# Performance work log

Measured on AMD Instinct MI355X. Metric: run time of the kernel, lower is better.

## Reference

```python
import jax, jax.numpy as jnp
import numpy as np
import math

B, S, D, H, FF = 2, 2048, 1024, 16, 4096
HD = D // H
EPS = 1e-5


def setup_inputs() -> dict:
    key = jax.random.key(0)
    ks = jax.random.split(key, 16)
    w = lambda k, shape: (jax.random.normal(k, shape, jnp.float32) * 0.02)
    future = jnp.triu(jnp.ones((S, S), dtype=bool), k=1)
    causal_mask = jnp.where(future, -jnp.inf, 0.0).astype(jnp.float32)
    return {
        "src": jax.random.normal(ks[0], (B, S, D), jnp.float32),
        "causal_mask": causal_mask,
        "Wq": w(ks[1], (D, D)), "bq": jnp.zeros((D,), jnp.float32),
        "Wk": w(ks[2], (D, D)), "bk": jnp.zeros((D,), jnp.float32),
        "Wv": w(ks[3], (D, D)), "bv": jnp.zeros((D,), jnp.float32),
        "Wo": w(ks[4], (D, D)), "bo": jnp.zeros((D,), jnp.float32),
        "W1": w(ks[5], (D, FF)), "b1": jnp.zeros((FF,), jnp.float32),
        "W2": w(ks[6], (FF, D)), "b2": jnp.zeros((D,), jnp.float32),
        "ln1_g": jnp.ones((D,), jnp.float32), "ln1_b": jnp.zeros((D,), jnp.float32),
        "ln2_g": jnp.ones((D,), jnp.float32), "ln2_b": jnp.zeros((D,), jnp.float32),
    }


def _layernorm(x, g, b):
    mu = jnp.mean(x, axis=-1, keepdims=True)
    var = jnp.mean((x - mu) ** 2, axis=-1, keepdims=True)
    return (x - mu) * jax.lax.rsqrt(var + EPS) * g + b


def reference(src, causal_mask, Wq, bq, Wk, bk, Wv, bv, Wo, bo,
              W1, b1, W2, b2, ln1_g, ln1_b, ln2_g, ln2_b):
    # QKV projections, split heads: [B,S,D] -> [B,H,S,HD]
    def split_heads(x):
        return x.reshape(B, S, H, HD).transpose(0, 2, 1, 3)

    q = split_heads(src @ Wq + bq)
    k = split_heads(src @ Wk + bk)
    v = split_heads(src @ Wv + bv)

    # scores: [B,H,S,S]; attn_mask = causal_mask broadcast over batch, then head dim
    scores = jnp.einsum("bhqd,bhkd->bhqk", q, k) / math.sqrt(HD)
    scores = scores + causal_mask[None, None, :, :]
    # scores[scores != scores] = 0
    scores = jnp.where(jnp.isnan(scores), 0.0, scores)
    # rows that are entirely inf -> 0
    mask_all_inf = jnp.all(jnp.isinf(scores), axis=-1, keepdims=True)
    scores = jnp.where(mask_all_inf, 0.0, scores)
    attn = jax.nn.softmax(scores, axis=-1)
    attn = jnp.where(jnp.isnan(attn), 0.0, attn)

    ctx = jnp.einsum("bhqk,bhkd->bhqd", attn, v)
    ctx = ctx.transpose(0, 2, 1, 3).reshape(B, S, D)
    attn_out = ctx @ Wo + bo

    x = _layernorm(src + attn_out, ln1_g, ln1_b)
    ff = jax.nn.relu(x @ W1 + b1) @ W2 + b2
    return _layernorm(x + ff, ln2_g, ln2_b)
```

## Files before the change

### kernel.cpp

```cpp
#include <hip/hip_runtime.h>

#define SS 2048
#define DD 1024
#define HH 16
#define HDIM 64
#define BB 2
#define FFD 4096
#define MR (BB*SS)
#define QKVLD 3072

typedef __bf16 bf16;
typedef __bf16 bf16x4 __attribute__((ext_vector_type(4)));
typedef __bf16 bf16x8 __attribute__((ext_vector_type(8)));
typedef float f32x4 __attribute__((ext_vector_type(4)));

struct P4 { bf16* p[4]; };

__device__ inline f32x4 mfma32(bf16x8 a, bf16x8 b, f32x4 c) {
  return __builtin_amdgcn_mfma_f32_16x16x32_bf16(a, b, c, 0, 0, 0);
}

__device__ inline void gload_lds16(const void* g, void* l) {
  __builtin_amdgcn_global_load_lds(
      (const __attribute__((address_space(1))) void*)g,
      (__attribute__((address_space(3))) void*)l, 16, 0, 0);
}

__global__ __launch_bounds__(256)
void cvt_bf16_kernel(const float* __restrict__ in, bf16* __restrict__ out, int n) {
  int i = (blockIdx.x * 256 + threadIdx.x) * 4;
  if (i >= n) return;
  float4 v = *(const float4*)(in + i);
  bf16x4 o;
  o[0] = (bf16)v.x; o[1] = (bf16)v.y; o[2] = (bf16)v.z; o[3] = (bf16)v.w;
  *(bf16x4*)(out + i) = o;
}

__global__ __launch_bounds__(256)
void concat_bias_kernel(const float* __restrict__ bq, const float* __restrict__ bk,
                        const float* __restrict__ bv, float* __restrict__ out) {
  int i = blockIdx.x * 256 + threadIdx.x;
  out[i] = i < 1024 ? bq[i] : (i < 2048 ? bk[i - 1024] : bv[i - 2048]);
}

__global__ __launch_bounds__(256)
void transpose_w_kernel(const float* __restrict__ W, bf16* __restrict__ Wt,
                        int K, int N) {
  __shared__ float t[32][33];
  int tx = threadIdx.x & 31, ty = threadIdx.x >> 5;
  int n0 = blockIdx.x * 32, k0 = blockIdx.y * 32;
  #pragma unroll
  for (int i = 0; i < 4; ++i)
    t[ty + i*8][tx] = W[(size_t)(k0 + ty + i*8) * N + n0 + tx];
  __syncthreads();
  #pragma unroll
  for (int i = 0; i < 4; ++i)
    Wt[(size_t)(n0 + ty + i*8) * K + k0 + tx] = (bf16)t[tx][ty + i*8];
}

__global__ __launch_bounds__(256)
void transpose_v_kernel(const bf16* __restrict__ V2d, bf16* __restrict__ Vt) {
  __shared__ bf16 t[32][33];
  int tx = threadIdx.x & 31, ty = threadIdx.x >> 5;
  int s0 = blockIdx.x * 32, d0 = blockIdx.y * 32;
  int bh = blockIdx.z;
  int b = bh >> 4, h = bh & 15;
  #pragma unroll
  for (int i = 0; i < 4; ++i)
    t[ty + i*8][tx] = V2d[(size_t)(b*SS + s0 + ty + i*8) * QKVLD + h*HDIM + d0 + tx];
  __syncthreads();
  #pragma unroll
  for (int i = 0; i < 4; ++i)
    Vt[((size_t)bh*HDIM + d0 + ty + i*8) * SS + s0 + tx] = t[tx][ty + i*8];
}

template<int OUT_BF16, int RELU, int SPLITK>
__global__ __launch_bounds__(512)
void gemm256(const bf16* __restrict__ A, const bf16* __restrict__ Bt,
             const float* __restrict__ bias, void* __restrict__ Cout,
             P4 part, int Ndim, int Kdim) {
  __shared__ bf16 Asm[2][256 * 64];
  __shared__ bf16 Bsm[2][256 * 64];
  const int gx = gridDim.x, gy = gridDim.y;
  const int gxy = gx * gy;
  const int nwg = gxy * gridDim.z;
  const int lin = (blockIdx.z * gy + blockIdx.y) * gx + blockIdx.x;
  const int swz = (lin & 7) * (nwg >> 3) + (lin >> 3);
  int bz = 0, rem = swz;
  if (SPLITK > 1) { bz = swz / gxy; rem = swz - bz * gxy; }
  const int by = rem / gx, bx = rem - by * gx;
  const int m0 = by * 256, n0 = bx * 256;
  const int tid = threadIdx.x;
  const int wave = tid >> 6, lane = tid & 63;
  const int g = lane >> 4, r = lane & 15;
  const int wr = wave >> 2, wn = wave & 3;
  const int kstart = bz * (Kdim / SPLITK);

  const int srow = wave * 8 + (lane >> 3);
  const int skslot = (lane & 7) ^ (lane >> 3);
  const bf16* Ag = A + (size_t)(m0 + srow) * Kdim + kstart + skslot * 8;
  const bf16* Bg = Bt + (size_t)(n0 + srow) * Kdim + kstart + skslot * 8;

  f32x4 acc[8][4] = {};
  const int NT = (Kdim / SPLITK) >> 6;

  auto stage = [&](int t) {
    const int kb = t << 6;
    bf16* Ad = Asm[t & 1];
    bf16* Bd = Bsm[t & 1];
    #pragma unroll
    for (int j = 0; j < 4; ++j)
      gload_lds16(Ag + (size_t)j * 64 * Kdim + kb, Ad + (j * 64 + wave * 8) * 64);
    #pragma unroll
    for (int j = 0; j < 4; ++j)
      gload_lds16(Bg + (size_t)j * 64 * Kdim + kb, Bd + (j * 64 + wave * 8) * 64);
  };

  stage(0);
  asm volatile("s_waitcnt vmcnt(0)" ::: "memory");
  asm volatile("s_barrier" ::: "memory");

  for (int t = 0; t < NT; ++t) {
    const bf16* Ab = Asm[t & 1];
    const bf16* Bb = Bsm[t & 1];
    #pragma unroll
    for (int ph = 0; ph < 4; ++ph) {
      const int mq = ph >> 1, nq = ph & 1;
      bf16x8 af[4][2], bfr[2][2];
      #pragma unroll
      for (int i = 0; i < 4; ++i) {
        const int row = wr * 128 + (mq * 4 + i) * 16 + r;
        #pragma unroll
        for (int kk = 0; kk < 2; ++kk)
          af[i][kk] = *(const bf16x8*)(Ab + row * 64 + (((kk * 4 + g) ^ (r & 7)) * 8));
      }
      #pragma unroll
      for (int i = 0; i < 2; ++i) {
        const int rowb = wn * 64 + (nq * 2 + i) * 16 + r;
        #pragma unroll
        for (int kk = 0; kk < 2; ++kk)
          bfr[i][kk] = *(const bf16x8*)(Bb + rowb * 64 + (((kk * 4 + g) ^ (r & 7)) * 8));
      }
      if (ph == 0 && t + 1 < NT) stage(t + 1);
      asm volatile("s_barrier" ::: "memory");
      __builtin_amdgcn_s_setprio(1);
      #pragma unroll
      for (int i = 0; i < 4; ++i)
        #pragma unroll
        for (int jn = 0; jn < 2; ++jn)
          #pragma unroll
          for (int kk = 0; kk < 2; ++kk)
            acc[mq * 4 + i][nq * 2 + jn] =
                mfma32(af[i][kk], bfr[jn][kk], acc[mq * 4 + i][nq * 2 + jn]);
      __builtin_amdgcn_s_setprio(0);
      asm volatile("s_barrier" ::: "memory");
    }
    asm volatile("s_waitcnt vmcnt(0)" ::: "memory");
    asm volatile("s_barrier" ::: "memory");
  }

  #pragma unroll
  for (int mi = 0; mi < 8; ++mi) {
    #pragma unroll
    for (int ni = 0; ni < 4; ++ni) {
      const int col = n0 + wn * 64 + ni * 16 + r;
      const float bv = (SPLITK > 1) ? 0.f : bias[col];
      #pragma unroll
      for (int jj = 0; jj < 4; ++jj) {
        const int row = m0 + wr * 128 + mi * 16 + g * 4 + jj;
        float v = acc[mi][ni][jj] + bv;
        if (RELU) v = fmaxf(v, 0.f);
        if (SPLITK > 1) part.p[bz][(size_t)row * Ndim + col] = (bf16)v;
        else if (OUT_BF16) ((bf16*)Cout)[(size_t)row * Ndim + col] = (bf16)v;
        else               ((float*)Cout)[(size_t)row * Ndim + col] = v;
      }
    }
  }
}

template<int OUT_BF16, int RELU, int SPLITK>
__global__ __launch_bounds__(256)
void gemm_bt(const bf16* __restrict__ A, const bf16* __restrict__ Bt,
             const float* __restrict__ bias, void* __restrict__ Cout,
             float* __restrict__ Cout2, int Mdim, int Ndim, int Kdim) {
  __shared__ bf16 As[128 * 32];
  __shared__ bf16 Bs[128 * 32];
  const int gx = gridDim.x, gy = gridDim.y;
  const int nwg = gx * gy * gridDim.z;
  const int lin = (blockIdx.z * gy + blockIdx.y) * gx + blockIdx.x;
  const int swz = (lin & 7) * (nwg >> 3) + (lin >> 3);
  const int bz = swz / (gx * gy);
  const int rem = swz - bz * gx * gy;
  const int by = rem / gx;
  const int bx = rem - by * gx;
  const int tid = threadIdx.x;
  const int wave = tid >> 6;
  const int lane = tid & 63;
  const int g = lane >> 4;
  const int r = lane & 15;
  const int m0 = by * 128;
  const int n0 = bx * 128;
  const int kchunk = Kdim / SPLITK;
  const int kstart = bz * kchunk;
  const int wr = wave >> 1, wc = wave & 1;
  f32x4 acc[4][4] = {};
  const int strow = tid >> 2;
  const int stcol = (tid & 3) * 8;
  const bf16* Abase = A + (size_t)(m0 + strow) * Kdim + kstart + stcol;
  const bf16* Bbase = Bt + (size_t)(n0 + strow) * Kdim + kstart + stcol;
  bf16* AsW = As + wave * 512;
  bf16* BsW = Bs + wave * 512;
  for (int k0 = 0; k0 < kchunk; k0 += 32) {
    __syncthreads();
    gload_lds16(Abase + k0, AsW);
    gload_lds16(Abase + k0 + (size_t)64 * Kdim, AsW + 2048);
    gload_lds16(Bbase + k0, BsW);
    gload_lds16(Bbase + k0 + (size_t)64 * Kdim, BsW + 2048);
    __syncthreads();
    bf16x8 af[4], bfr[4];
    #pragma unroll
    for (int i = 0; i < 4; ++i)
      af[i] = *(const bf16x8*)(As + (wr*64 + i*16 + r) * 32 + g * 8);
    #pragma unroll
    for (int i = 0; i < 4; ++i)
      bfr[i] = *(const bf16x8*)(Bs + (wc*64 + i*16 + r) * 32 + g * 8);
    #pragma unroll
    for (int mi = 0; mi < 4; ++mi)
      #pragma unroll
      for (int ni = 0; ni < 4; ++ni)
        acc[mi][ni] = mfma32(af[mi], bfr[ni], acc[mi][ni]);
  }
  float* outp = (SPLITK > 1 && bz) ? Cout2 : (float*)Cout;
  #pragma unroll
  for (int mi = 0; mi < 4; ++mi) {
    #pragma unroll
    for (int ni = 0; ni < 4; ++ni) {
      const int col = n0 + wc*64 + ni*16 + r;
      const float bv = (SPLITK > 1) ? 0.f : bias[col];
      #pragma unroll
      for (int j = 0; j < 4; ++j) {
        const int row = m0 + wr*64 + mi*16 + g*4 + j;
        float v = acc[mi][ni][j] + bv;
        if (RELU) v = fmaxf(v, 0.f);
        if (OUT_BF16) ((bf16*)Cout)[(size_t)row * Ndim + col] = (bf16)v;
        else          outp[(size_t)row * Ndim + col] = v;
      }
    }
  }
}

__global__ __launch_bounds__(256)
void attn_kernel(const bf16* __restrict__ Q2d, const bf16* __restrict__ K2d,
                 const bf16* __restrict__ Vt, bf16* __restrict__ ctx) {
  __shared__ bf16 Ks[2 * 4096];
  __shared__ bf16 Vs[2 * 4096];
  const int tid = threadIdx.x;
  const int wave = tid >> 6;
  const int lane = tid & 63;
  const int g = lane >> 4, r = lane & 15;
  const int lin = blockIdx.y * gridDim.x + blockIdx.x;
  const int swz = (lin & 7) * 64 + (lin >> 3);
  const int p = swz & 15;
  const int bh = swz >> 4;
  const int b = bh >> 4, h = bh & 15;

  const int strow = wave * 16 + (lane >> 2);
  const int lslot = (lane & 3) ^ ((lane >> 3) & 3);
  const bf16* srcK0 = K2d + (size_t)(b*SS + strow) * QKVLD + h*HDIM + lslot * 8;
  const bf16* srcK1 = srcK0 + 32;
  const bf16* srcV0 = Vt + ((size_t)bh*HDIM + strow) * SS + lslot * 8;
  const bf16* srcV1 = srcV0 + 32;

  auto sw = [](int row, int s) { return row * 32 + ((s ^ ((row >> 1) & 3)) * 8); };

  const int kr0 = 8 * (r >> 2) + (r & 3);
  const int oKa0 = sw(kr0,      g), oKb0 = 2048 + oKa0;
  const int oKa1 = sw(kr0 +  4, g), oKb1 = 2048 + oKa1;
  const int oKa2 = sw(kr0 + 32, g), oKb2 = 2048 + oKa2;
  const int oKa3 = sw(kr0 + 36, g), oKb3 = 2048 + oKa3;
  int oV[4];
  #pragma unroll
  for (int c = 0; c < 4; ++c) oV[c] = sw(c * 16 + r, g);

  const float K2 = 0.18033688f;

  #pragma unroll
  for (int tt = 0; tt < 2; ++tt) {
    const int tile = tt ? (31 - p) : p;
    const int q0 = tile * 64 + wave * 16;
    const int qg = q0 + r;
    const bf16* qp = Q2d + (size_t)(b*SS + q0 + r) * QKVLD + h * HDIM;
    const bf16x8 qf0 = *(const bf16x8*)(qp + g * 8);
    const bf16x8 qf1 = *(const bf16x8*)(qp + 32 + g * 8);
    f32x4 ov[4] = {};
    float m2 = 0.f, l = 0.f;
    const int nst = tile + 1;
    {
      bf16* kb = Ks + wave * 512;
      bf16* vb = Vs + wave * 512;
      gload_lds16(srcK0, kb);
      gload_lds16(srcK1, kb + 2048);
      gload_lds16(srcV0, vb);
      gload_lds16(srcV1, vb + 2048);
    }
    __syncthreads();
    int cur = 0;
    for (int st = 0; st < nst; ++st) {
      const int k0 = st * 64;
      if (st + 1 < nst) {
        const int kn = k0 + 64;
        bf16* kb = Ks + (cur ^ 1) * 4096 + wave * 512;
        bf16* vb = Vs + (cur ^ 1) * 4096 + wave * 512;
        gload_lds16(srcK0 + (size_t)kn * QKVLD, kb);
        gload_lds16(srcK1 + (size_t)kn * QKVLD, kb + 2048);
        gload_lds16(srcV0 + kn, vb);
        gload_lds16(srcV1 + kn, vb + 2048);
      }
      const bf16* Kb = Ks + cur * 4096;
      const bf16* Vb = Vs + cur * 4096;
      f32x4 c0 = {}, c1 = {}, c2 = {}, c3 = {};
      __builtin_amdgcn_s_setprio(1);
      c0 = mfma32(*(const bf16x8*)(Kb + oKa0), qf0, c0);
      c1 = mfma32(*(const bf16x8*)(Kb + oKa1), qf0, c1);
      c2 = mfma32(*(const bf16x8*)(Kb + oKa2), qf0, c2);
      c3 = mfma32(*(const bf16x8*)(Kb + oKa3), qf0, c3);
      c0 = mfma32(*(const bf16x8*)(Kb + oKb0), qf1, c0);
      c1 = mfma32(*(const bf16x8*)(Kb + oKb1), qf1, c1);
      c2 = mfma32(*(const bf16x8*)(Kb + oKb2), qf1, c2);
      c3 = mfma32(*(const bf16x8*)(Kb + oKb3), qf1, c3);
      __builtin_amdgcn_s_setprio(0);
      float f0[4], f1[4], f2[4], f3[4];
      float tmax = -3.0e38f;
      const bool need_mask = (k0 + 63 > qg);
      #pragma unroll
      for (int j = 0; j < 4; ++j) {
        float s0 = fmaf(c0[j], K2, -m2);
        float s1 = fmaf(c1[j], K2, -m2);
        float s2 = fmaf(c2[j], K2, -m2);
        float s3 = fmaf(c3[j], K2, -m2);
        if (need_mask) {
          if (k0 + 8*g + j > qg)          s0 = -3.0e38f;
          if (k0 + 8*g + 4 + j > qg)      s1 = -3.0e38f;
          if (k0 + 32 + 8*g + j > qg)     s2 = -3.0e38f;
          if (k0 + 32 + 8*g + 4 + j > qg) s3 = -3.0e38f;
        }
        f0[j] = s0; f1[j] = s1; f2[j] = s2; f3[j] = s3;
        tmax = fmaxf(tmax, fmaxf(fmaxf(s0, s1), fmaxf(s2, s3)));
      }
      tmax = fmaxf(tmax, __shfl_xor(tmax, 16));
      tmax = fmaxf(tmax, __shfl_xor(tmax, 32));
      if (__any(tmax > 11.54f)) {
        const float rmp = fmaxf(tmax, 0.f);
        m2 += rmp;
        const float sc = exp2f(-rmp);
        l *= sc;
        #pragma unroll
        for (int j = 0; j < 4; ++j) {
          f0[j] -= rmp; f1[j] -= rmp; f2[j] -= rmp; f3[j] -= rmp;
          const float scj = __shfl(sc, 4*g + j);
          #pragma unroll
          for (int c = 0; c < 4; ++c) ov[c][j] *= scj;
        }
      }
      float tsum = 0.f;
      float p0[4], p1[4], p2[4], p3[4];
      #pragma unroll
      for (int j = 0; j < 4; ++j) {
        p0[j] = exp2f(f0[j]);
        p1[j] = exp2f(f1[j]);
        p2[j] = exp2f(f2[j]);
        p3[j] = exp2f(f3[j]);
        tsum += (p0[j] + p1[j]) + (p2[j] + p3[j]);
      }
      tsum += __shfl_xor(tsum, 16);
      tsum += __shfl_xor(tsum, 32);
      l += tsum;
      bf16x8 pfa, pfb;
      #pragma unroll
      for (int j = 0; j < 4; ++j) {
        pfa[j] = (bf16)p0[j]; pfa[4 + j] = (bf16)p1[j];
        pfb[j] = (bf16)p2[j]; pfb[4 + j] = (bf16)p3[j];
      }
      __builtin_amdgcn_s_setprio(1);
      #pragma unroll
      for (int c = 0; c < 4; ++c) {
        bf16x8 vfa = *(const bf16x8*)(Vb + oV[c]);
        bf16x8 vfb = *(const bf16x8*)(Vb + 2048 + oV[c]);
        ov[c] = mfma32(pfa, vfa, ov[c]);
        ov[c] = mfma32(pfb, vfb, ov[c]);
      }
      __builtin_amdgcn_s_setprio(0);
      __syncthreads();
      cur ^= 1;
    }
    #pragma unroll
    for (int j = 0; j < 4; ++j) {
      const float lj = __shfl(l, 4*g + j);
      const float inv = 1.f / lj;
      const int row = b*SS + q0 + 4*g + j;
      #pragma unroll
      for (int c = 0; c < 4; ++c)
        ctx[(size_t)row * DD + h*HDIM + c*16 + r] = (bf16)(ov[c][j] * inv);
    }
  }
}

template<int NP, int HASB, int WRITEB>
__global__ __launch_bounds__(256)
void ln_kernel(const float* __restrict__ a, const float* __restrict__ p0,
               const float* __restrict__ p1, const float* __restrict__ cb,
               const float* __restrict__ gam, const float* __restrict__ bet,
               float* __restrict__ outf, bf16* __restrict__ outb) {
  const int row = blockIdx.x;
  const int tid = threadIdx.x;
  const size_t base = (size_t)row * DD + tid * 4;
  float4 va = *(const float4*)(a + base);
  float4 vc = *(const float4*)(p0 + base);
  float x0 = va.x + vc.x, x1 = va.y + vc.y, x2 = va.z + vc.z, x3 = va.w + vc.w;
  if (NP > 1) {
    float4 vp = *(const float4*)(p1 + base);
    x0 += vp.x; x1 += vp.y; x2 += vp.z; x3 += vp.w;
  }
  if (HASB) {
    float4 vb4 = *(const float4*)(cb + tid * 4);
    x0 += vb4.x; x1 += vb4.y; x2 += vb4.z; x3 += vb4.w;
  }
  float s  = x0 + x1 + x2 + x3;
  float s2 = x0*x0 + x1*x1 + x2*x2 + x3*x3;
  #pragma unroll
  for (int off = 32; off > 0; off >>= 1) {
    s  += __shfl_xor(s,  off);
    s2 += __shfl_xor(s2, off);
  }
  __shared__ float red[8];
  const int wv = tid >> 6;
  if ((tid & 63) == 0) { red[wv] = s; red[wv + 4] = s2; }
  __syncthreads();
  s  = red[0] + red[1] + red[2] + red[3];
  s2 = red[4] + red[5] + red[6] + red[7];
  const float mu  = s * (1.f / DD);
  const float var = s2 * (1.f / DD) - mu * mu;
  const float rs  = rsqrtf(var + 1e-5f);
  float4 vg = *(const float4*)(gam + tid * 4);
  float4 vb = *(const float4*)(bet + tid * 4);
  float y0 = (x0 - mu) * rs * vg.x + vb.x;
  float y1 = (x1 - mu) * rs * vg.y + vb.y;
  float y2 = (x2 - mu) * rs * vg.z + vb.z;
  float y3 = (x3 - mu) * rs * vg.w + vb.w;
  float4 yo; yo.x = y0; yo.y = y1; yo.z = y2; yo.w = y3;
  *(float4*)(outf + base) = yo;
  if (WRITEB) {
    bf16x4 ob;
    ob[0] = (bf16)y0; ob[1] = (bf16)y1; ob[2] = (bf16)y2; ob[3] = (bf16)y3;
    *(bf16x4*)(outb + base) = ob;
  }
}

__global__ __launch_bounds__(256)
void ln_bf4_kernel(const float* __restrict__ a, P4 part, const float* __restrict__ cb,
                   const float* __restrict__ gam, const float* __restrict__ bet,
                   float* __restrict__ outf) {
  const int row = blockIdx.x;
  const int tid = threadIdx.x;
  const size_t base = (size_t)row * DD + tid * 4;
  float4 va = *(const float4*)(a + base);
  bf16x4 u0 = *(const bf16x4*)(part.p[0] + base);
  bf16x4 u1 = *(const bf16x4*)(part.p[1] + base);
  bf16x4 u2 = *(const bf16x4*)(part.p[2] + base);
  bf16x4 u3 = *(const bf16x4*)(part.p[3] + base);
  float4 vb4 = *(const float4*)(cb + tid * 4);
  float x0 = va.x + ((float)u0[0] + (float)u1[0]) + ((float)u2[0] + (float)u3[0]) + vb4.x;
  float x1 = va.y + ((float)u0[1] + (float)u1[1]) + ((float)u2[1] + (float)u3[1]) + vb4.y;
  float x2 = va.z + ((float)u0[2] + (float)u1[2]) + ((float)u2[2] + (float)u3[2]) + vb4.z;
  float x3 = va.w + ((float)u0[3] + (float)u1[3]) + ((float)u2[3] + (float)u3[3]) + vb4.w;
  float s  = x0 + x1 + x2 + x3;
  float s2 = x0*x0 + x1*x1 + x2*x2 + x3*x3;
  #pragma unroll
  for (int off = 32; off > 0; off >>= 1) {
    s  += __shfl_xor(s,  off);
    s2 += __shfl_xor(s2, off);
  }
  __shared__ float red[8];
  const int wv = tid >> 6;
  if ((tid & 63) == 0) { red[wv] = s; red[wv + 4] = s2; }
  __syncthreads();
  s  = red[0] + red[1] + red[2] + red[3];
  s2 = red[4] + red[5] + red[6] + red[7];
  const float mu  = s * (1.f / DD);
  const float var = s2 * (1.f / DD) - mu * mu;
  const float rs  = rsqrtf(var + 1e-5f);
  float4 vg = *(const float4*)(gam + tid * 4);
  float4 vb = *(const float4*)(bet + tid * 4);
  float4 yo;
  yo.x = (x0 - mu) * rs * vg.x + vb.x;
  yo.y = (x1 - mu) * rs * vg.y + vb.y;
  yo.z = (x2 - mu) * rs * vg.z + vb.z;
  yo.w = (x3 - mu) * rs * vg.w + vb.w;
  *(float4*)(outf + base) = yo;
}

extern "C" void kernel_launch(void* const* d_in, const int* in_sizes, int n_in,
                              void* d_out, int out_size, void* d_ws, size_t ws_size,
                              hipStream_t stream) {
  const float* src  = (const float*)d_in[0];
  const float* Wq   = (const float*)d_in[2];
  const float* bq   = (const float*)d_in[3];
  const float* Wk   = (const float*)d_in[4];
  const float* bk   = (const float*)d_in[5];
  const float* Wv   = (const float*)d_in[6];
  const float* bv   = (const float*)d_in[7];
  const float* Wo   = (const float*)d_in[8];
  const float* bo   = (const float*)d_in[9];
  const float* W1   = (const float*)d_in[10];
  const float* b1   = (const float*)d_in[11];
  const float* W2   = (const float*)d_in[12];
  const float* b2   = (const float*)d_in[13];
  const float* ln1g = (const float*)d_in[14];
  const float* ln1b = (const float*)d_in[15];
  const float* ln2g = (const float*)d_in[16];
  const float* ln2b = (const float*)d_in[17];

  char* ws = (char*)d_ws;
  const size_t MB = 1024 * 1024;
  bf16* wqkvt = (bf16*)(ws + 0 * MB);
  bf16* wot   = (bf16*)(ws + 6 * MB);
  bf16* w1t   = (bf16*)(ws + 8 * MB);
  bf16* w2t   = (bf16*)(ws + 16 * MB);
  bf16* bsrc  = (bf16*)(ws + 24 * MB);
  bf16* xb    = bsrc;
  bf16* qkv   = (bf16*)(ws + 32 * MB);
  bf16* vt    = (bf16*)(ws + 56 * MB);
  bf16* ctx   = (bf16*)(ws + 64 * MB);
  bf16* ff1   = qkv;
  float* xf   = (float*)(ws + 72 * MB);
  float* bqkv = (float*)(ws + 88 * MB);
  float* wo_p1 = (float*)(ws + 32 * MB);
  float* attn_out = (float*)d_out;
  float* outp  = (float*)d_out;
  P4 fp;
  fp.p[0] = (bf16*)(ws + 0 * MB);
  fp.p[1] = (bf16*)(ws + 8 * MB);
  fp.p[2] = (bf16*)(ws + 24 * MB);
  fp.p[3] = (bf16*)(ws + 64 * MB);

  cvt_bf16_kernel<<<(MR * DD) / 1024, 256, 0, stream>>>(src, bsrc, MR * DD);
  transpose_w_kernel<<<dim3(32, 32), 256, 0, stream>>>(Wq, wqkvt,             DD, DD);
  transpose_w_kernel<<<dim3(32, 32), 256, 0, stream>>>(Wk, wqkvt + 1024*1024, DD, DD);
  transpose_w_kernel<<<dim3(32, 32), 256, 0, stream>>>(Wv, wqkvt + 2048*1024, DD, DD);
  transpose_w_kernel<<<dim3(32, 32), 256, 0, stream>>>(Wo, wot, DD, DD);
  transpose_w_kernel<<<dim3(128, 32), 256, 0, stream>>>(W1, w1t, DD, FFD);
  transpose_w_kernel<<<dim3(32, 128), 256, 0, stream>>>(W2, w2t, FFD, DD);
  concat_bias_kernel<<<12, 256, 0, stream>>>(bq, bk, bv, bqkv);

  gemm256<1, 0, 1><<<dim3(QKVLD / 256, MR / 256), 512, 0, stream>>>(bsrc, wqkvt, bqkv, qkv, P4{}, QKVLD, DD);
  transpose_v_kernel<<<dim3(SS / 32, HDIM / 32, BB * HH), 256, 0, stream>>>(qkv + 2048, vt);

  attn_kernel<<<dim3(16, BB * HH), 256, 0, stream>>>(qkv, qkv + 1024, vt, ctx);

  gemm_bt<0, 0, 2><<<dim3(8, 32, 2), 256, 0, stream>>>(ctx, wot, nullptr, attn_out, wo_p1, MR, DD, DD);
  ln_kernel<2, 1, 1><<<MR, 256, 0, stream>>>(src, attn_out, wo_p1, bo, ln1g, ln1b, xf, xb);

  gemm256<1, 1, 1><<<dim3(FFD / 256, MR / 256), 512, 0, stream>>>(xb, w1t, b1, ff1, P4{}, FFD, DD);
  gemm256<0, 0, 4><<<dim3(DD / 256, MR / 256, 4), 512, 0, stream>>>(ff1, w2t, nullptr, nullptr, fp, DD, FFD);
  ln_bf4_kernel<<<MR, 256, 0, stream>>>(xf, fp, b2, ln2g, ln2b, outp);
}
```

Before: 258.8 us.

## Use split-K gemm256 for Wo projection, batch weight transposes, fast exp2

The output projection moves from the 128-tile gemm_bt with 2-way split-K to the 256-tile gemm256 with 4-way split-K, writing bf16 partials that a templated LN kernel sums. The four square weight transposes are merged into one launch using a z-indexed pointer table. Attention softmax uses the hardware v_exp_f32 instruction instead of exp2f. Risks include extra bf16 rounding on the partials and fewer workgroups for the Wo GEMM (64 tiles times 4 splits).

Measured after the change: 252.2 us. 1.03x faster.

```diff
diff --git a/kernel.cpp b/kernel.cpp
--- a/kernel.cpp
+++ b/kernel.cpp
@@ -15,6 +15,7 @@
 typedef float f32x4 __attribute__((ext_vector_type(4)));
 
 struct P4 { bf16* p[4]; };
+struct TP4 { const float* src[4]; bf16* dst[4]; };
 
 __device__ inline f32x4 mfma32(bf16x8 a, bf16x8 b, f32x4 c) {
   return __builtin_amdgcn_mfma_f32_16x16x32_bf16(a, b, c, 0, 0, 0);
@@ -24,6 +25,19 @@
   __builtin_amdgcn_global_load_lds(
       (const __attribute__((address_space(1))) void*)g,
       (__attribute__((address_space(3))) void*)l, 16, 0, 0);
+}
+
+#if defined(__has_builtin)
+#if __has_builtin(__builtin_amdgcn_exp2f)
+#define HAVE_EXP2_BUILTIN 1
+#endif
+#endif
+__device__ inline float fast_exp2(float x) {
+#ifdef HAVE_EXP2_BUILTIN
+  return __builtin_amdgcn_exp2f(x);
+#else
+  float r; asm("v_exp_f32 %0, %1" : "=v"(r) : "v"(x)); return r;
+#endif
 }
 
 __global__ __launch_bounds__(256)
@@ -41,6 +55,22 @@
                         const float* __restrict__ bv, float* __restrict__ out) {
   int i = blockIdx.x * 256 + threadIdx.x;
   out[i] = i < 1024 ? bq[i] : (i < 2048 ? bk[i - 1024] : bv[i - 2048]);
+}
+
+__global__ __launch_bounds__(256)
+void transpose_w4_kernel(TP4 t) {
+  __shared__ float tl[32][33];
+  const float* W = t.src[blockIdx.z];
+  bf16* Wt = t.dst[blockIdx.z];
+  int tx = threadIdx.x & 31, ty = threadIdx.x >> 5;
+  int n0 = blockIdx.x * 32, k0 = blockIdx.y * 32;
+  #pragma unroll
+  for (int i = 0; i < 4; ++i)
+    tl[ty + i*8][tx] = W[(size_t)(k0 + ty + i*8) * DD + n0 + tx];
+  __syncthreads();
+  #pragma unroll
+  for (int i = 0; i < 4; ++i)
+    Wt[(size_t)(n0 + ty + i*8) * DD + k0 + tx] = (bf16)tl[tx][ty + i*8];
 }
 
 __global__ __launch_bounds__(256)
@@ -173,77 +203,6 @@
         if (SPLITK > 1) part.p[bz][(size_t)row * Ndim + col] = (bf16)v;
         else if (OUT_BF16) ((bf16*)Cout)[(size_t)row * Ndim + col] = (bf16)v;
         else               ((float*)Cout)[(size_t)row * Ndim + col] = v;
-      }
-    }
-  }
-}
-
-template<int OUT_BF16, int RELU, int SPLITK>
-__global__ __launch_bounds__(256)
-void gemm_bt(const bf16* __restrict__ A, const bf16* __restrict__ Bt,
-             const float* __restrict__ bias, void* __restrict__ Cout,
-             float* __restrict__ Cout2, int Mdim, int Ndim, int Kdim) {
-  __shared__ bf16 As[128 * 32];
-  __shared__ bf16 Bs[128 * 32];
-  const int gx = gridDim.x, gy = gridDim.y;
-  const int nwg = gx * gy * gridDim.z;
-  const int lin = (blockIdx.z * gy + blockIdx.y) * gx + blockIdx.x;
-  const int swz = (lin & 7) * (nwg >> 3) + (lin >> 3);
-  const int bz = swz / (gx * gy);
-  const int rem = swz - bz * gx * gy;
-  const int by = rem / gx;
-  const int bx = rem - by * gx;
-  const int tid = threadIdx.x;
-  const int wave = tid >> 6;
-  const int lane = tid & 63;
-  const int g = lane >> 4;
-  const int r = lane & 15;
-  const int m0 = by * 128;
-  const int n0 = bx * 128;
-  const int kchunk = Kdim / SPLITK;
-  const int kstart = bz * kchunk;
-  const int wr = wave >> 1, wc = wave & 1;
-  f32x4 acc[4][4] = {};
-  const int strow = tid >> 2;
-  const int stcol = (tid & 3) * 8;
-  const bf16* Abase = A + (size_t)(m0 + strow) * Kdim + kstart + stcol;
-  const bf16* Bbase = Bt + (size_t)(n0 + strow) * Kdim + kstart + stcol;
-  bf16* AsW = As + wave * 512;
-  bf16* BsW = Bs + wave * 512;
-  for (int k0 = 0; k0 < kchunk; k0 += 32) {
-    __syncthreads();
-    gload_lds16(Abase + k0, AsW);
-    gload_lds16(Abase + k0 + (size_t)64 * Kdim, AsW + 2048);
-    gload_lds16(Bbase + k0, BsW);
-    gload_lds16(Bbase + k0 + (size_t)64 * Kdim, BsW + 2048);
-    __syncthreads();
-    bf16x8 af[4], bfr[4];
-    #pragma unroll
-    for (int i = 0; i < 4; ++i)
-      af[i] = *(const bf16x8*)(As + (wr*64 + i*16 + r) * 32 + g * 8);
-    #pragma unroll
-    for (int i = 0; i < 4; ++i)
-      bfr[i] = *(const bf16x8*)(Bs + (wc*64 + i*16 + r) * 32 + g * 8);
-    #pragma unroll
-    for (int mi = 0; mi < 4; ++mi)
-      #pragma unroll
-      for (int ni = 0; ni < 4; ++ni)
-        acc[mi][ni] = mfma32(af[mi], bfr[ni], acc[mi][ni]);
-  }
-  float* outp = (SPLITK > 1 && bz) ? Cout2 : (float*)Cout;
-  #pragma unroll
-  for (int mi = 0; mi < 4; ++mi) {
-    #pragma unroll
-    for (int ni = 0; ni < 4; ++ni) {
-      const int col = n0 + wc*64 + ni*16 + r;
-      const float bv = (SPLITK > 1) ? 0.f : bias[col];
-      #pragma unroll
-      for (int j = 0; j < 4; ++j) {
-        const int row = m0 + wr*64 + mi*16 + g*4 + j;
-        float v = acc[mi][ni][j] + bv;
-        if (RELU) v = fmaxf(v, 0.f);
-        if (OUT_BF16) ((bf16*)Cout)[(size_t)row * Ndim + col] = (bf16)v;
-        else          outp[(size_t)row * Ndim + col] = v;
       }
     }
   }
@@ -352,7 +311,7 @@
       if (__any(tmax > 11.54f)) {
         const float rmp = fmaxf(tmax, 0.f);
         m2 += rmp;
-        const float sc = exp2f(-rmp);
+        const float sc = fast_exp2(-rmp);
         l *= sc;
         #pragma unroll
         for (int j = 0; j < 4; ++j) {
@@ -366,10 +325,10 @@
       float p0[4], p1[4], p2[4], p3[4];
       #pragma unroll
       for (int j = 0; j < 4; ++j) {
-        p0[j] = exp2f(f0[j]);
-        p1[j] = exp2f(f1[j]);
-        p2[j] = exp2f(f2[j]);
-        p3[j] = exp2f(f3[j]);
+        p0[j] = fast_exp2(f0[j]);
+        p1[j] = fast_exp2(f1[j]);
+        p2[j] = fast_exp2(f2[j]);
+        p3[j] = fast_exp2(f3[j]);
         tsum += (p0[j] + p1[j]) + (p2[j] + p3[j]);
       }
       tsum += __shfl_xor(tsum, 16);
@@ -405,26 +364,24 @@
   }
 }
 
-template<int NP, int HASB, int WRITEB>
-__global__ __launch_bounds__(256)
-void ln_kernel(const float* __restrict__ a, const float* __restrict__ p0,
-               const float* __restrict__ p1, const float* __restrict__ cb,
-               const float* __restrict__ gam, const float* __restrict__ bet,
-               float* __restrict__ outf, bf16* __restrict__ outb) {
+template<int WRITEB>
+__global__ __launch_bounds__(256)
+void ln_bf4_kernel(const float* __restrict__ a, P4 part, const float* __restrict__ cb,
+                   const float* __restrict__ gam, const float* __restrict__ bet,
+                   float* __restrict__ outf, bf16* __restrict__ outb) {
   const int row = blockIdx.x;
   const int tid = threadIdx.x;
   const size_t base = (size_t)row * DD + tid * 4;
   float4 va = *(const float4*)(a + base);
-  float4 vc = *(const float4*)(p0 + base);
-  float x0 = va.x + vc.x, x1 = va.y + vc.y, x2 = va.z + vc.z, x3 = va.w + vc.w;
-  if (NP > 1) {
-    float4 vp = *(const float4*)(p1 + base);
-    x0 += vp.x; x1 += vp.y; x2 += vp.z; x3 += vp.w;
-  }
-  if (HASB) {
-    float4 vb4 = *(const float4*)(cb + tid * 4);
-    x0 += vb4.x; x1 += vb4.y; x2 += vb4.z; x3 += vb4.w;
-  }
+  bf16x4 u0 = *(const bf16x4*)(part.p[0] + base);
+  bf16x4 u1 = *(const bf16x4*)(part.p[1] + base);
+  bf16x4 u2 = *(const bf16x4*)(part.p[2] + base);
+  bf16x4 u3 = *(const bf16x4*)(part.p[3] + base);
+  float4 vb4 = *(const float4*)(cb + tid * 4);
+  float x0 = va.x + ((float)u0[0] + (float)u1[0]) + ((float)u2[0] + (float)u3[0]) + vb4.x;
+  float x1 = va.y + ((float)u0[1] + (float)u1[1]) + ((float)u2[1] + (float)u3[1]) + vb4.y;
+  float x2 = va.z + ((float)u0[2] + (float)u1[2]) + ((float)u2[2] + (float)u3[2]) + vb4.z;
+  float x3 = va.w + ((float)u0[3] + (float)u1[3]) + ((float)u2[3] + (float)u3[3]) + vb4.w;
   float s  = x0 + x1 + x2 + x3;
   float s2 = x0*x0 + x1*x1 + x2*x2 + x3*x3;
   #pragma unroll
@@ -456,49 +413,6 @@
   }
 }
 
-__global__ __launch_bounds__(256)
-void ln_bf4_kernel(const float* __restrict__ a, P4 part, const float* __restrict__ cb,
-                   const float* __restrict__ gam, const float* __restrict__ bet,
-                   float* __restrict__ outf) {
-  const int row = blockIdx.x;
-  const int tid = threadIdx.x;
-  const size_t base = (size_t)row * DD + tid * 4;
-  float4 va = *(const float4*)(a + base);
-  bf16x4 u0 = *(const bf16x4*)(part.p[0] + base);
-  bf16x4 u1 = *(const bf16x4*)(part.p[1] + base);
-  bf16x4 u2 = *(const bf16x4*)(part.p[2] + base);
-  bf16x4 u3 = *(const bf16x4*)(part.p[3] + base);
-  float4 vb4 = *(const float4*)(cb + tid * 4);
-  float x0 = va.x + ((float)u0[0] + (float)u1[0]) + ((float)u2[0] + (float)u3[0]) + vb4.x;
-  float x1 = va.y + ((float)u0[1] + (float)u1[1]) + ((float)u2[1] + (float)u3[1]) + vb4.y;
-  float x2 = va.z + ((float)u0[2] + (float)u1[2]) + ((float)u2[2] + (float)u3[2]) + vb4.z;
-  float x3 = va.w + ((float)u0[3] + (float)u1[3]) + ((float)u2[3] + (float)u3[3]) + vb4.w;
-  float s  = x0 + x1 + x2 + x3;
-  float s2 = x0*x0 + x1*x1 + x2*x2 + x3*x3;
-  #pragma unroll
-  for (int off = 32; off > 0; off >>= 1) {
-    s  += __shfl_xor(s,  off);
-    s2 += __shfl_xor(s2, off);
-  }
-  __shared__ float red[8];
-  const int wv = tid >> 6;
-  if ((tid & 63) == 0) { red[wv] = s; red[wv + 4] = s2; }
-  __syncthreads();
-  s  = red[0] + red[1] + red[2] + red[3];
-  s2 = red[4] + red[5] + red[6] + red[7];
-  const float mu  = s * (1.f / DD);
-  const float var = s2 * (1.f / DD) - mu * mu;
-  const float rs  = rsqrtf(var + 1e-5f);
-  float4 vg = *(const float4*)(gam + tid * 4);
-  float4 vb = *(const float4*)(bet + tid * 4);
-  float4 yo;
-  yo.x = (x0 - mu) * rs * vg.x + vb.x;
-  yo.y = (x1 - mu) * rs * vg.y + vb.y;
-  yo.z = (x2 - mu) * rs * vg.z + vb.z;
-  yo.w = (x3 - mu) * rs * vg.w + vb.w;
-  *(float4*)(outf + base) = yo;
-}
-
 extern "C" void kernel_launch(void* const* d_in, const int* in_sizes, int n_in,
                               void* d_out, int out_size, void* d_ws, size_t ws_size,
                               hipStream_t stream) {
@@ -534,9 +448,13 @@
   bf16* ff1   = qkv;
   float* xf   = (float*)(ws + 72 * MB);
   float* bqkv = (float*)(ws + 88 * MB);
-  float* wo_p1 = (float*)(ws + 32 * MB);
-  float* attn_out = (float*)d_out;
-  float* outp  = (float*)d_out;
+  float* outp = (float*)d_out;
+
+  P4 wop;
+  wop.p[0] = (bf16*)(ws + 32 * MB);
+  wop.p[1] = (bf16*)(ws + 40 * MB);
+  wop.p[2] = (bf16*)(ws + 48 * MB);
+  wop.p[3] = (bf16*)(ws + 56 * MB);
   P4 fp;
   fp.p[0] = (bf16*)(ws + 0 * MB);
   fp.p[1] = (bf16*)(ws + 8 * MB);
@@ -544,10 +462,12 @@
   fp.p[3] = (bf16*)(ws + 64 * MB);
 
   cvt_bf16_kernel<<<(MR * DD) / 1024, 256, 0, stream>>>(src, bsrc, MR * DD);
-  transpose_w_kernel<<<dim3(32, 32), 256, 0, stream>>>(Wq, wqkvt,             DD, DD);
-  transpose_w_kernel<<<dim3(32, 32), 256, 0, stream>>>(Wk, wqkvt + 1024*1024, DD, DD);
-  transpose_w_kernel<<<dim3(32, 32), 256, 0, stream>>>(Wv, wqkvt + 2048*1024, DD, DD);
-  transpose_w_kernel<<<dim3(32, 32), 256, 0, stream>>>(Wo, wot, DD, DD);
+  TP4 tp;
+  tp.src[0] = Wq; tp.dst[0] = wqkvt;
+  tp.src[1] = Wk; tp.dst[1] = wqkvt + 1024*1024;
+  tp.src[2] = Wv; tp.dst[2] = wqkvt + 2048*1024;
+  tp.src[3] = Wo; tp.dst[3] = wot;
+  transpose_w4_kernel<<<dim3(32, 32, 4), 256, 0, stream>>>(tp);
   transpose_w_kernel<<<dim3(128, 32), 256, 0, stream>>>(W1, w1t, DD, FFD);
   transpose_w_kernel<<<dim3(32, 128), 256, 0, stream>>>(W2, w2t, FFD, DD);
   concat_bias_kernel<<<12, 256, 0, stream>>>(bq, bk, bv, bqkv);
@@ -557,10 +477,10 @@
 
   attn_kernel<<<dim3(16, BB * HH), 256, 0, stream>>>(qkv, qkv + 1024, vt, ctx);
 
-  gemm_bt<0, 0, 2><<<dim3(8, 32, 2), 256, 0, stream>>>(ctx, wot, nullptr, attn_out, wo_p1, MR, DD, DD);
-  ln_kernel<2, 1, 1><<<MR, 256, 0, stream>>>(src, attn_out, wo_p1, bo, ln1g, ln1b, xf, xb);
+  gemm256<0, 0, 4><<<dim3(DD / 256, MR / 256, 4), 512, 0, stream>>>(ctx, wot, nullptr, nullptr, wop, DD, DD);
+  ln_bf4_kernel<1><<<MR, 256, 0, stream>>>(src, wop, bo, ln1g, ln1b, xf, xb);
 
   gemm256<1, 1, 1><<<dim3(FFD / 256, MR / 256), 512, 0, stream>>>(xb, w1t, b1, ff1, P4{}, FFD, DD);
   gemm256<0, 0, 4><<<dim3(DD / 256, MR / 256, 4), 512, 0, stream>>>(ff1, w2t, nullptr, nullptr, fp, DD, FFD);
-  ln_bf4_kernel<<<MR, 256, 0, stream>>>(xf, fp, b2, ln2g, ln2b, outp);
-}
+  ln_bf4_kernel<0><<<MR, 256, 0, stream>>>(xf, fp, b2, ln2g, ln2b, outp, nullptr);
+}
```
